# Optimization experiments

Measured on AMD Instinct MI355X. Metric: run time of the kernel, lower is better.

## Reference

```python
import jax, jax.numpy as jnp
import numpy as np

EMBED = 256; HEADS = 8; LEVELS = 4; POINTS = 4; DIM = EMBED // HEADS


def _bilinear_gather(vflat, H, W, px, py):
    """grid_sample(mode='bilinear', padding='zeros', align_corners=False).
    vflat: (bs, heads, H*W, d); px, py: (bs, heads, nq, P) pixel coords.
    Returns (bs, heads, nq, P, d).
    """
    x0 = jnp.floor(px); y0 = jnp.floor(py)
    x1 = x0 + 1.0;      y1 = y0 + 1.0
    wx1 = px - x0; wx0 = 1.0 - wx1
    wy1 = py - y0; wy0 = 1.0 - wy1

    def corner(ix, iy, w):
        valid = (ix >= 0) & (ix <= W - 1) & (iy >= 0) & (iy <= H - 1)
        idx = (jnp.clip(iy, 0, H - 1) * W + jnp.clip(ix, 0, W - 1)).astype(jnp.int32)
        b, h, nq, P = idx.shape
        g = jnp.take_along_axis(vflat, idx.reshape(b, h, nq * P)[..., None], axis=2)
        g = g.reshape(b, h, nq, P, -1)
        return g * (w * valid)[..., None]

    return (corner(x0, y0, wx0 * wy0) + corner(x1, y0, wx1 * wy0)
            + corner(x0, y1, wx0 * wy1) + corner(x1, y1, wx1 * wy1))


def _ms_deform_attn(value4, shapes, loc, attn):
    """value4 (bs,nv,heads,D); loc (bs,nq,heads,L,P,2) in [0,1];
    attn (bs,nq,heads,L,P). Returns (bs,nq,heads*D)."""
    bs, nq = loc.shape[0], loc.shape[1]
    grids = 2.0 * loc - 1.0
    attn_t = jnp.transpose(attn, (0, 2, 1, 3, 4))  # (bs,heads,nq,L,P)
    out = jnp.zeros((bs, HEADS, nq, DIM), value4.dtype)
    start = 0
    for lvl in range(LEVELS):
        H, W = int(shapes[lvl, 0]), int(shapes[lvl, 1])
        v = value4[:, start:start + H * W]                 # (bs,HW,heads,D)
        vflat = jnp.transpose(v, (0, 2, 1, 3))             # (bs,heads,HW,D)
        g = jnp.transpose(grids[:, :, :, lvl], (0, 2, 1, 3, 4))  # (bs,heads,nq,P,2)
        px = (g[..., 0] + 1.0) * (W * 0.5) - 0.5
        py = (g[..., 1] + 1.0) * (H * 0.5) - 0.5
        sampled = _bilinear_gather(vflat, H, W, px, py)    # (bs,heads,nq,P,D)
        out = out + jnp.einsum('bhqpd,bhqp->bhqd', sampled, attn_t[:, :, :, lvl])
        start += H * W
    return jnp.transpose(out, (0, 2, 1, 3)).reshape(bs, nq, HEADS * DIM)


def _forward(query, value, query_pos, reference_points, last_reference_offsets,
             shapes, Wv, bv, Wo, bo, Wa, ba, Wout, bout):
    identity = query
    q = query + query_pos
    bs, nq, _ = q.shape
    nv = value.shape[1]
    v = (value @ Wv + bv).reshape(bs, nv, HEADS, DIM)
    off = (q @ Wo + bo).reshape(bs, nq, HEADS, LEVELS, POINTS, 2)
    attn = jax.nn.softmax((q @ Wa + ba).reshape(bs, nq, HEADS, LEVELS * POINTS), axis=-1)
    attn = attn.reshape(bs, nq, HEADS, LEVELS, POINTS)
    wh = jnp.asarray(np.asarray(shapes)[:, ::-1].copy(), jnp.float32)  # (L,2) as (w,h)
    loc = (reference_points[:, :, None, :, None, :]
           + off / wh[None, None, None, :, None, :]
           + last_reference_offsets[:, :, :, None, None, :])  # flow-guided per-head shift
    out = _ms_deform_attn(v, shapes, loc, attn)
    return out @ Wout + bout + identity  # dropout is identity at eval


def setup_inputs() -> dict:
    key = jax.random.key(0)
    ks = jax.random.split(key, 10)
    bs, nq = 8, 1200
    shapes = np.array([[92, 160], [46, 80], [23, 40], [12, 20]], np.int64)
    nv = int((shapes[:, 0] * shapes[:, 1]).sum())
    f = jnp.float32
    return {
        "query": jax.random.normal(ks[0], (bs, nq, EMBED), f),
        "value": jax.random.normal(ks[1], (bs, nv, EMBED), f),
        "query_pos": jax.random.normal(ks[2], (bs, nq, EMBED), f),
        "reference_points": jax.random.uniform(ks[3], (bs, nq, LEVELS, 2), f),
        "last_reference_offsets": jax.random.normal(ks[4], (bs, nq, HEADS, 2), f) * 0.02,
        "spatial_shapes": shapes,
        "Wv": jax.random.normal(ks[5], (EMBED, EMBED), f) * 0.02,
        "bv": jnp.zeros((EMBED,), f),
        "Wo": jax.random.normal(ks[6], (EMBED, HEADS * LEVELS * POINTS * 2), f) * 0.02,
        "bo": jax.random.normal(ks[7], (HEADS * LEVELS * POINTS * 2,), f) * 0.02,
        "Wa": jax.random.normal(ks[8], (EMBED, HEADS * LEVELS * POINTS), f) * 0.02,
        "ba": jnp.zeros((HEADS * LEVELS * POINTS,), f),
        "Wout": jax.random.normal(ks[9], (EMBED, EMBED), f) * 0.02,
        "bout": jnp.zeros((EMBED,), f),
    }


def reference(query, value, query_pos, reference_points, last_reference_offsets,
              spatial_shapes, Wv, bv, Wo, bo, Wa, ba, Wout, bout):
    return _forward(query, value, query_pos, reference_points, last_reference_offsets,
                    spatial_shapes, Wv, bv, Wo, bo, Wa, ba, Wout, bout)
```

## Files before the change

### kernel.cpp

```cpp
#include <hip/hip_runtime.h>
#include <math.h>

#define BS 8
#define NQ 1200
#define NV 19560
#define NVP 19584
#define EMB 256
#define TPB 153

typedef __bf16 bf16;
typedef bf16 bf16x8 __attribute__((ext_vector_type(8)));
typedef bf16 bf16x4 __attribute__((ext_vector_type(4)));
typedef float f32x4 __attribute__((ext_vector_type(4)));

static __device__ __forceinline__ bf16x8 cvt8(float4 a, float4 b) {
    bf16x8 r;
    r[0] = (bf16)a.x; r[1] = (bf16)a.y; r[2] = (bf16)a.z; r[3] = (bf16)a.w;
    r[4] = (bf16)b.x; r[5] = (bf16)b.y; r[6] = (bf16)b.z; r[7] = (bf16)b.w;
    return r;
}

static __device__ __forceinline__ void gl16(const void* g, void* l) {
    __builtin_amdgcn_global_load_lds(
        (const __attribute__((address_space(1))) void*)g,
        (__attribute__((address_space(3))) void*)l, 16, 0, 0);
}

__global__ __launch_bounds__(256) void prep_k(
    const float* __restrict__ Wv, const float* __restrict__ Wo,
    const float* __restrict__ Wa, const float* __restrict__ Wout,
    const float* __restrict__ query, const float* __restrict__ qpos,
    const float* __restrict__ bo, const float* __restrict__ ba,
    bf16* __restrict__ Wv_p, bf16* __restrict__ Wo_p,
    bf16* __restrict__ Wa_p, bf16* __restrict__ Wout_p,
    bf16* __restrict__ qsum, float* __restrict__ cb)
{
    int bid = blockIdx.x, tid = threadIdx.x;
    if (bid < 896) {
        const float* src; bf16* dst; int N, t0;
        if (bid < 256)      { src = Wv;   dst = Wv_p;   N = 256; t0 = bid * 256; }
        else if (bid < 512) { src = Wo;   dst = Wo_p;   N = 256; t0 = (bid - 256) * 256; }
        else if (bid < 640) { src = Wa;   dst = Wa_p;   N = 128; t0 = (bid - 512) * 256; }
        else                { src = Wout; dst = Wout_p; N = 256; t0 = (bid - 640) * 256; }
        int t = t0 + tid;
        int n = t >> 8, k = t & 255;
        dst[t] = (bf16)src[k * N + n];
    } else if (bid < 10496) {
        int t = (bid - 896) * 256 + tid;
        qsum[t] = (bf16)(query[t] + qpos[t]);
    } else {
        cb[tid] = bo[tid];
        if (tid < 128) cb[256 + tid] = ba[tid];
    }
}

__global__ __launch_bounds__(256, 1) void vgemm_k(
    const float* __restrict__ A, const bf16* __restrict__ Bp,
    const float* __restrict__ bias, bf16* __restrict__ outB, int Mtiles)
{
    __shared__ __align__(16) bf16  sB[256 * 256];
    __shared__ __align__(16) float sA[4 * 2 * 1024];
    const int tid = threadIdx.x;
    const int lane = tid & 63;
    const int w = tid >> 6;
    const int l16 = lane & 15;
    const int qd = lane >> 4;

#pragma unroll
    for (int i = 0; i < 32; ++i) {
        int s = i * 256 + tid;
        int r = s >> 5, p = s & 31, c = p ^ (r & 7);
        gl16(Bp + (size_t)r * 256 + c * 8, sB + ((size_t)i * 256 + w * 64) * 8);
    }

    float* sAw = sA + w * 2048;
    const int arow = lane >> 3;
    const int aslot = (lane & 7) ^ arow;
    auto stageT = [&](int t_, int kg, int buf) {
        int b_ = t_ / TPB, p0_ = (t_ - b_ * TPB) * 128;
#pragma unroll
        for (int i = 0; i < 4; ++i) {
            int pix = min(p0_ + w * 32 + i * 8 + arow, NV - 1);
            gl16(A + ((size_t)b_ * NV + pix) * 256 + kg * 32 + aslot * 4,
                 sAw + buf * 1024 + i * 256);
        }
    };

    int t = blockIdx.x;
    stageT(t, 0, 0);
    stageT(t, 1, 1);

    f32x4 bias4[16];
#pragma unroll
    for (int ct = 0; ct < 16; ++ct)
        bias4[ct] = *(const f32x4*)(bias + ct * 16 + qd * 4);

    __syncthreads();

    const int akey = l16 & 7;
    f32x4 acc0[16], acc1[16];

    auto compute = [&](int kg, int buf) {
        const float* ab = sAw + buf * 1024;
        const float* ar0 = ab + l16 * 32;
        const float* ar1 = ab + (16 + l16) * 32;
        float4 a00 = *(const float4*)(ar0 + ((qd * 2    ) ^ akey) * 4);
        float4 a01 = *(const float4*)(ar0 + ((qd * 2 + 1) ^ akey) * 4);
        float4 a10 = *(const float4*)(ar1 + ((qd * 2    ) ^ akey) * 4);
        float4 a11 = *(const float4*)(ar1 + ((qd * 2 + 1) ^ akey) * 4);
        bf16x8 af0 = cvt8(a00, a01);
        bf16x8 af1 = cvt8(a10, a11);
#pragma unroll
        for (int ct = 0; ct < 16; ++ct) {
            int brow = ct * 16 + l16;
            bf16x8 bfr = *(const bf16x8*)(sB + (size_t)brow * 256 +
                                          ((kg * 4 + qd) ^ (brow & 7)) * 8);
            acc0[ct] = __builtin_amdgcn_mfma_f32_16x16x32_bf16(bfr, af0, acc0[ct], 0, 0, 0);
            acc1[ct] = __builtin_amdgcn_mfma_f32_16x16x32_bf16(bfr, af1, acc1[ct], 0, 0, 0);
        }
    };

#define VM_WAIT36 asm volatile("s_waitcnt vmcnt(36)" ::: "memory")
#define VM_WAIT4  asm volatile("s_waitcnt vmcnt(4)"  ::: "memory")

    while (true) {
#pragma unroll
        for (int ct = 0; ct < 16; ++ct) { acc0[ct] = bias4[ct]; acc1[ct] = bias4[ct]; }

        int tn = t + gridDim.x;
        const bool last = (tn >= Mtiles);

        VM_WAIT36; compute(0, 0); stageT(t, 2, 0);
        VM_WAIT36; compute(1, 1); stageT(t, 3, 1);
        VM_WAIT4;  compute(2, 0); stageT(t, 4, 0);
        VM_WAIT4;  compute(3, 1); stageT(t, 5, 1);
        VM_WAIT4;  compute(4, 0); stageT(t, 6, 0);
        VM_WAIT4;  compute(5, 1); stageT(t, 7, 1);
        VM_WAIT4;  compute(6, 0); if (!last) stageT(tn, 0, 0);
        VM_WAIT4;  compute(7, 1); if (!last) stageT(tn, 1, 1);

        int b = t / TPB, p0 = (t - b * TPB) * 128;
        int pix0 = p0 + w * 32 + l16;
#pragma unroll
        for (int ct = 0; ct < 16; ++ct) {
            bf16* dst = outB + ((size_t)(b * 8 + (ct >> 1)) * NVP) * 32
                             + (ct & 1) * 16 + qd * 4;
            bf16x4 v0, v1;
#pragma unroll
            for (int r = 0; r < 4; ++r) { v0[r] = (bf16)acc0[ct][r]; v1[r] = (bf16)acc1[ct][r]; }
            *(bf16x4*)(dst + (size_t)pix0 * 32)        = v0;
            *(bf16x4*)(dst + (size_t)(pix0 + 16) * 32) = v1;
        }

        if (last) break;
        t = tn;
    }
#undef VM_WAIT36
#undef VM_WAIT4
}

template <int NS, int NB, int NGRP, bool HAS_RES, bool OUT_BF16>
__global__ __launch_bounds__(256, 2) void gemm3_k(
    const bf16* __restrict__ Ah, const bf16* __restrict__ Bp,
    const float* __restrict__ bias, const float* __restrict__ res,
    float* __restrict__ outF, bf16* __restrict__ outB, int Mtiles)
{
    constexpr int CT = NB / 16;
    __shared__ __align__(16) bf16 sB[NB * 256];
    const int tid = threadIdx.x;
    const int lane = tid & 63;
    const int w = tid >> 6;
    const int l16 = lane & 15;
    const int qd = lane >> 4;
    const int col0 = (blockIdx.x % NGRP) * NB;
    const int tstride = gridDim.x / NGRP;
    const bf16* Bsrc = Bp + (size_t)col0 * 256;

    uint4 curH[8], nxtH[8];
    auto loadA = [&](int t, uint4* dH) {
        size_t rb = ((size_t)t * 64 + w * 16 + l16) * 256;
#pragma unroll
        for (int kc = 0; kc < 8; ++kc)
            dH[kc] = *(const uint4*)(Ah + rb + kc * 32 + qd * 8);
    };

    int tile = blockIdx.x / NGRP;
    if (tile < Mtiles) loadA(tile, curH);

#pragma unroll
    for (int i = 0; i < NB * 32 / 256; ++i) {
        int s = i * 256 + tid;
        int r = s >> 5, p = s & 31, c = p ^ (r & 7);
        gl16(Bsrc + (size_t)r * 256 + c * 8, sB + (size_t)(i * 256 + w * 64) * 8);
    }
    __syncthreads();

    for (; tile < Mtiles; tile += tstride) {
        int nt = tile + tstride;
        if (nt < Mtiles) loadA(nt, nxtH);

        f32x4 acc[CT];
#pragma unroll
        for (int c = 0; c < CT; ++c) acc[c] = (f32x4){0.f, 0.f, 0.f, 0.f};
#pragma unroll
        for (int kc = 0; kc < 8; ++kc) {
            bf16x8 af = *(const bf16x8*)&curH[kc];
#pragma unroll
            for (int ct = 0; ct < CT; ++ct) {
                int brow = ct * 16 + l16;
                int chunk = (kc * 4 + qd) ^ (l16 & 7);
                bf16x8 bfr = *(const bf16x8*)(sB + (size_t)brow * 256 + chunk * 8);
                acc[ct] = __builtin_amdgcn_mfma_f32_16x16x32_bf16(af, bfr, acc[ct], 0, 0, 0);
            }
        }
#pragma unroll
        for (int ct = 0; ct < CT; ++ct) {
            int col = col0 + ct * 16 + l16;
            float bbv = bias[col];
#pragma unroll
            for (int r = 0; r < 4; ++r) {
                int row = tile * 64 + w * 16 + qd * 4 + r;
                size_t idx = (size_t)row * NS + col;
                float v = acc[ct][r] + bbv;
                if (HAS_RES) v += res[(size_t)row * 256 + col];
                if (OUT_BF16) outB[idx] = (bf16)v;
                else          outF[idx] = v;
            }
        }
#pragma unroll
        for (int i = 0; i < 8; ++i) curH[i] = nxtH[i];
    }
}

static __device__ __forceinline__ void b8f(uint4 u, float* f) {
    f[0] = __uint_as_float(u.x << 16); f[1] = __uint_as_float(u.x & 0xffff0000u);
    f[2] = __uint_as_float(u.y << 16); f[3] = __uint_as_float(u.y & 0xffff0000u);
    f[4] = __uint_as_float(u.z << 16); f[5] = __uint_as_float(u.z & 0xffff0000u);
    f[6] = __uint_as_float(u.w << 16); f[7] = __uint_as_float(u.w & 0xffff0000u);
}

__global__ __launch_bounds__(256) void sample4_k(
    const bf16* __restrict__ vv, const float* __restrict__ comb,
    const float* __restrict__ refp, const float* __restrict__ lref,
    bf16* __restrict__ outb)
{
    const int cH[4] = {92, 46, 23, 12};
    const int cW[4] = {160, 80, 40, 20};
    const int cS[4] = {0, 14720, 18400, 19320};
    const int w = threadIdx.x >> 6;
    const int lane = threadIdx.x & 63;
    const int wid = blockIdx.x * 4 + w;
    const int bq = wid >> 3, h = wid & 7;
    const int b = bq / NQ;
    const int ps = lane >> 3;
    const int dg8 = lane & 7;
    const int hx2 = dg8 >> 2;

    float lg0 = comb[(size_t)bq * 384 + 256 + h * 16 + ps];
    float lg1 = comb[(size_t)bq * 384 + 256 + h * 16 + 8 + ps];
    float mx = fmaxf(lg0, lg1);
#pragma unroll
    for (int s = 8; s < 64; s <<= 1) mx = fmaxf(mx, __shfl_xor(mx, s));
    float e0 = __expf(lg0 - mx), e1 = __expf(lg1 - mx);
    float ss = e0 + e1;
#pragma unroll
    for (int s = 8; s < 64; s <<= 1) ss += __shfl_xor(ss, s);
    float inv = 1.f / ss;

    float acc[8];
#pragma unroll
    for (int j = 0; j < 8; j++) acc[j] = 0.f;

    const float* rp = refp + (size_t)bq * 8;
    float lrx = lref[(size_t)bq * 16 + h * 2];
    float lry = lref[(size_t)bq * 16 + h * 2 + 1];

#pragma unroll
    for (int s2 = 0; s2 < 2; ++s2) {
        int p = s2 * 8 + ps;
        int lvl = p >> 2;
        const int Hh = cH[lvl], Ww = cW[lvl];
        float ox = comb[(size_t)bq * 384 + h * 32 + p * 2];
        float oy = comb[(size_t)bq * 384 + h * 32 + p * 2 + 1];
        float rx = rp[lvl * 2], ry = rp[lvl * 2 + 1];

        float px = (rx + ox / (float)Ww + lrx) * (float)Ww - 0.5f;
        float py = (ry + oy / (float)Hh + lry) * (float)Hh - 0.5f;
        float x0f = floorf(px), y0f = floorf(py);
        int x0 = (int)x0f, y0 = (int)y0f;
        float wx1 = px - x0f, wx0 = 1.f - wx1;
        float wy1 = py - y0f, wy0 = 1.f - wy1;
        bool xa = (unsigned)x0 < (unsigned)Ww, xb = (unsigned)(x0 + 1) < (unsigned)Ww;
        bool ya = (unsigned)y0 < (unsigned)Hh, yb = (unsigned)(y0 + 1) < (unsigned)Hh;
        int px0 = min(max(x0, 0), Ww - 2);
        int hx = px0 + hx2;
        float wxh = (hx == x0 && xa) ? wx0 : ((hx == x0 + 1 && xb) ? wx1 : 0.f);
        int yc0 = min(max(y0, 0), Hh - 1), yc1 = min(max(y0 + 1, 0), Hh - 1);
        float wgt = (s2 ? e1 : e0) * inv;
        float wA = wgt * wy0 * (ya ? 1.f : 0.f) * wxh;
        float wB = wgt * wy1 * (yb ? 1.f : 0.f) * wxh;

        const bf16* base = vv + ((size_t)(b * 8 + h) * NVP + cS[lvl]) * 32 + dg8 * 8;
        uint4 gA = *(const uint4*)(base + ((size_t)yc0 * Ww + px0) * 32);
        uint4 gB = *(const uint4*)(base + ((size_t)yc1 * Ww + px0) * 32);

        float f[8];
        b8f(gA, f);
#pragma unroll
        for (int j = 0; j < 8; j++) acc[j] = fmaf(wA, f[j], acc[j]);
        b8f(gB, f);
#pragma unroll
        for (int j = 0; j < 8; j++) acc[j] = fmaf(wB, f[j], acc[j]);
    }

#pragma unroll
    for (int s = 4; s < 64; s <<= 1)
#pragma unroll
        for (int j = 0; j < 8; j++) acc[j] += __shfl_xor(acc[j], s);

    if (lane < 4) {
        bf16x8 o;
#pragma unroll
        for (int j = 0; j < 8; j++) o[j] = (bf16)acc[j];
        *(bf16x8*)(outb + (size_t)bq * 256 + h * 32 + lane * 8) = o;
    }
}

extern "C" void kernel_launch(void* const* d_in, const int* in_sizes, int n_in,
                              void* d_out, int out_size, void* d_ws, size_t ws_size,
                              hipStream_t stream) {
    (void)in_sizes; (void)n_in; (void)out_size; (void)ws_size;
    const float* query = (const float*)d_in[0];
    const float* value = (const float*)d_in[1];
    const float* qpos  = (const float*)d_in[2];
    const float* refp  = (const float*)d_in[3];
    const float* lref  = (const float*)d_in[4];
    const float* Wv   = (const float*)d_in[6];
    const float* bv   = (const float*)d_in[7];
    const float* Wo   = (const float*)d_in[8];
    const float* bo   = (const float*)d_in[9];
    const float* Wa   = (const float*)d_in[10];
    const float* ba   = (const float*)d_in[11];
    const float* Wout = (const float*)d_in[12];
    const float* bout = (const float*)d_in[13];

    char* ws = (char*)d_ws;
    bf16*  Wv_p   = (bf16*)(ws + 0);
    bf16*  Wo_p   = (bf16*)(ws + 131072);
    bf16*  Wa_p   = (bf16*)(ws + 262144);
    bf16*  Wout_p = (bf16*)(ws + 327680);
    bf16*  qsum   = (bf16*)(ws + 458752);
    float* comb   = (float*)(ws + 5373952);
    bf16*  tsa_b  = (bf16*)(ws + 20119552);
    bf16*  v_b    = (bf16*)(ws + 25034752);
    float* cbias  = (float*)(ws + 105250816);

    prep_k<<<10497, 256, 0, stream>>>(Wv, Wo, Wa, Wout, query, qpos, bo, ba,
                                      Wv_p, Wo_p, Wa_p, Wout_p, qsum, cbias);

    vgemm_k<<<256, 256, 0, stream>>>(value, Wv_p, bv, v_b, BS * TPB);
    gemm3_k<384, 128, 3, false, false><<<450, 256, 0, stream>>>(
        qsum, Wo_p, cbias, nullptr, comb, nullptr, (BS * NQ) / 64);
    sample4_k<<<(BS * NQ * 8) / 4, 256, 0, stream>>>(v_b, comb, refp, lref, tsa_b);
    gemm3_k<256, 128, 2, true, false><<<300, 256, 0, stream>>>(
        tsa_b, Wout_p, bout, query, (float*)d_out, nullptr, (BS * NQ) / 64);
}
```

Baseline: 393.2 us.

## Replace persistent value GEMM with per-tile K-chunked blocks and tiled weight transpose

Measured after the change: 399.2 us. No clear change (+1.5%).

```diff
diff --git a/kernel.cpp b/kernel.cpp
--- a/kernel.cpp
+++ b/kernel.cpp
@@ -35,128 +35,135 @@
     bf16* __restrict__ Wa_p, bf16* __restrict__ Wout_p,
     bf16* __restrict__ qsum, float* __restrict__ cb)
 {
+    __shared__ float t64[64][65];
     int bid = blockIdx.x, tid = threadIdx.x;
-    if (bid < 896) {
-        const float* src; bf16* dst; int N, t0;
-        if (bid < 256)      { src = Wv;   dst = Wv_p;   N = 256; t0 = bid * 256; }
-        else if (bid < 512) { src = Wo;   dst = Wo_p;   N = 256; t0 = (bid - 256) * 256; }
-        else if (bid < 640) { src = Wa;   dst = Wa_p;   N = 128; t0 = (bid - 512) * 256; }
-        else                { src = Wout; dst = Wout_p; N = 256; t0 = (bid - 640) * 256; }
-        int t = t0 + tid;
-        int n = t >> 8, k = t & 255;
-        dst[t] = (bf16)src[k * N + n];
-    } else if (bid < 10496) {
-        int t = (bid - 896) * 256 + tid;
-        qsum[t] = (bf16)(query[t] + qpos[t]);
+    if (bid < 56) {
+        const float* src; bf16* dst; int N, tile;
+        if (bid < 16)      { src = Wv;   dst = Wv_p;   N = 256; tile = bid; }
+        else if (bid < 32) { src = Wo;   dst = Wo_p;   N = 256; tile = bid - 16; }
+        else if (bid < 40) { src = Wa;   dst = Wa_p;   N = 128; tile = bid - 32; }
+        else               { src = Wout; dst = Wout_p; N = 256; tile = bid - 40; }
+        int ntn = N >> 6;
+        int k0 = (tile / ntn) << 6, n0 = (tile % ntn) << 6;
+#pragma unroll
+        for (int j = 0; j < 16; ++j) {
+            int idx = j * 256 + tid;
+            int r = idx >> 6, c = idx & 63;
+            t64[r][c] = src[(size_t)(k0 + r) * N + n0 + c];
+        }
+        __syncthreads();
+#pragma unroll
+        for (int j = 0; j < 16; ++j) {
+            int idx = j * 256 + tid;
+            int rn = idx >> 6, ck = idx & 63;
+            dst[(size_t)(n0 + rn) * 256 + k0 + ck] = (bf16)t64[ck][rn];
+        }
+    } else if (bid < 1256) {
+        size_t base = (size_t)(bid - 56) * 2048 + tid * 8;
+        float4 a0 = *(const float4*)(query + base);
+        float4 a1 = *(const float4*)(query + base + 4);
+        float4 b0 = *(const float4*)(qpos + base);
+        float4 b1 = *(const float4*)(qpos + base + 4);
+        bf16x8 o;
+        o[0] = (bf16)(a0.x + b0.x); o[1] = (bf16)(a0.y + b0.y);
+        o[2] = (bf16)(a0.z + b0.z); o[3] = (bf16)(a0.w + b0.w);
+        o[4] = (bf16)(a1.x + b1.x); o[5] = (bf16)(a1.y + b1.y);
+        o[6] = (bf16)(a1.z + b1.z); o[7] = (bf16)(a1.w + b1.w);
+        *(bf16x8*)(qsum + base) = o;
     } else {
         cb[tid] = bo[tid];
         if (tid < 128) cb[256 + tid] = ba[tid];
     }
 }
 
-__global__ __launch_bounds__(256, 1) void vgemm_k(
+__global__ __launch_bounds__(256, 2) void vgemm_k(
     const float* __restrict__ A, const bf16* __restrict__ Bp,
-    const float* __restrict__ bias, bf16* __restrict__ outB, int Mtiles)
+    const float* __restrict__ bias, bf16* __restrict__ outB)
 {
-    __shared__ __align__(16) bf16  sB[256 * 256];
-    __shared__ __align__(16) float sA[4 * 2 * 1024];
+    __shared__ __align__(16) float sA[2][128 * 32];
+    __shared__ __align__(16) bf16  sB[2][256 * 32];
     const int tid = threadIdx.x;
     const int lane = tid & 63;
     const int w = tid >> 6;
     const int l16 = lane & 15;
     const int qd = lane >> 4;
-
-#pragma unroll
-    for (int i = 0; i < 32; ++i) {
-        int s = i * 256 + tid;
-        int r = s >> 5, p = s & 31, c = p ^ (r & 7);
-        gl16(Bp + (size_t)r * 256 + c * 8, sB + ((size_t)i * 256 + w * 64) * 8);
-    }
-
-    float* sAw = sA + w * 2048;
+    const int t = blockIdx.x;
+    const int b = t / TPB, p0 = (t - b * TPB) * 128;
+
     const int arow = lane >> 3;
-    const int aslot = (lane & 7) ^ arow;
-    auto stageT = [&](int t_, int kg, int buf) {
-        int b_ = t_ / TPB, p0_ = (t_ - b_ * TPB) * 128;
+    const int aslot = lane & 7;
+    auto stageA = [&](int kg, int buf) {
 #pragma unroll
         for (int i = 0; i < 4; ++i) {
-            int pix = min(p0_ + w * 32 + i * 8 + arow, NV - 1);
-            gl16(A + ((size_t)b_ * NV + pix) * 256 + kg * 32 + aslot * 4,
-                 sAw + buf * 1024 + i * 256);
+            int lr = w * 32 + i * 8 + arow;
+            int pix = min(p0 + lr, NV - 1);
+            int gs = aslot ^ arow;
+            gl16(A + ((size_t)b * NV + pix) * 256 + kg * 32 + gs * 4,
+                 (float*)sA[buf] + (w * 32 + i * 8) * 32);
         }
     };
-
-    int t = blockIdx.x;
-    stageT(t, 0, 0);
-    stageT(t, 1, 1);
-
-    f32x4 bias4[16];
-#pragma unroll
-    for (int ct = 0; ct < 16; ++ct)
-        bias4[ct] = *(const f32x4*)(bias + ct * 16 + qd * 4);
+    const int bcol = lane >> 2;
+    const int bslt = lane & 3;
+    auto stageB = [&](int kg, int buf) {
+#pragma unroll
+        for (int i = 0; i < 4; ++i) {
+            int c = w * 64 + i * 16 + bcol;
+            int key = (c ^ (c >> 2)) & 3;
+            gl16(Bp + (size_t)c * 256 + kg * 32 + (bslt ^ key) * 8,
+                 (bf16*)sB[buf] + (w * 64 + i * 16) * 32);
+        }
+    };
+
+    stageA(0, 0);
+    stageB(0, 0);
+
+    f32x4 acc0[16], acc1[16];
+#pragma unroll
+    for (int ct = 0; ct < 16; ++ct) {
+        f32x4 bb = *(const f32x4*)(bias + ct * 16 + qd * 4);
+        acc0[ct] = bb; acc1[ct] = bb;
+    }
 
     __syncthreads();
 
     const int akey = l16 & 7;
-    f32x4 acc0[16], acc1[16];
-
-    auto compute = [&](int kg, int buf) {
-        const float* ab = sAw + buf * 1024;
-        const float* ar0 = ab + l16 * 32;
-        const float* ar1 = ab + (16 + l16) * 32;
-        float4 a00 = *(const float4*)(ar0 + ((qd * 2    ) ^ akey) * 4);
-        float4 a01 = *(const float4*)(ar0 + ((qd * 2 + 1) ^ akey) * 4);
-        float4 a10 = *(const float4*)(ar1 + ((qd * 2    ) ^ akey) * 4);
-        float4 a11 = *(const float4*)(ar1 + ((qd * 2 + 1) ^ akey) * 4);
-        bf16x8 af0 = cvt8(a00, a01);
-        bf16x8 af1 = cvt8(a10, a11);
-#pragma unroll
-        for (int ct = 0; ct < 16; ++ct) {
-            int brow = ct * 16 + l16;
-            bf16x8 bfr = *(const bf16x8*)(sB + (size_t)brow * 256 +
-                                          ((kg * 4 + qd) ^ (brow & 7)) * 8);
-            acc0[ct] = __builtin_amdgcn_mfma_f32_16x16x32_bf16(bfr, af0, acc0[ct], 0, 0, 0);
-            acc1[ct] = __builtin_amdgcn_mfma_f32_16x16x32_bf16(bfr, af1, acc1[ct], 0, 0, 0);
-        }
-    };
-
-#define VM_WAIT36 asm volatile("s_waitcnt vmcnt(36)" ::: "memory")
-#define VM_WAIT4  asm volatile("s_waitcnt vmcnt(4)"  ::: "memory")
-
-    while (true) {
-#pragma unroll
-        for (int ct = 0; ct < 16; ++ct) { acc0[ct] = bias4[ct]; acc1[ct] = bias4[ct]; }
-
-        int tn = t + gridDim.x;
-        const bool last = (tn >= Mtiles);
-
-        VM_WAIT36; compute(0, 0); stageT(t, 2, 0);
-        VM_WAIT36; compute(1, 1); stageT(t, 3, 1);
-        VM_WAIT4;  compute(2, 0); stageT(t, 4, 0);
-        VM_WAIT4;  compute(3, 1); stageT(t, 5, 1);
-        VM_WAIT4;  compute(4, 0); stageT(t, 6, 0);
-        VM_WAIT4;  compute(5, 1); stageT(t, 7, 1);
-        VM_WAIT4;  compute(6, 0); if (!last) stageT(tn, 0, 0);
-        VM_WAIT4;  compute(7, 1); if (!last) stageT(tn, 1, 1);
-
-        int b = t / TPB, p0 = (t - b * TPB) * 128;
-        int pix0 = p0 + w * 32 + l16;
-#pragma unroll
-        for (int ct = 0; ct < 16; ++ct) {
-            bf16* dst = outB + ((size_t)(b * 8 + (ct >> 1)) * NVP) * 32
-                             + (ct & 1) * 16 + qd * 4;
-            bf16x4 v0, v1;
-#pragma unroll
-            for (int r = 0; r < 4; ++r) { v0[r] = (bf16)acc0[ct][r]; v1[r] = (bf16)acc1[ct][r]; }
-            *(bf16x4*)(dst + (size_t)pix0 * 32)        = v0;
-            *(bf16x4*)(dst + (size_t)(pix0 + 16) * 32) = v1;
-        }
-
-        if (last) break;
-        t = tn;
-    }
-#undef VM_WAIT36
-#undef VM_WAIT4
+    int buf = 0;
+#pragma unroll
+    for (int kc = 0; kc < 8; ++kc) {
+        if (kc < 7) { stageA(kc + 1, buf ^ 1); stageB(kc + 1, buf ^ 1); }
+        {
+            const float* ar0 = sA[buf] + (w * 32 + l16) * 32;
+            const float* ar1 = ar0 + 16 * 32;
+            float4 a00 = *(const float4*)(ar0 + ((qd * 2    ) ^ akey) * 4);
+            float4 a01 = *(const float4*)(ar0 + ((qd * 2 + 1) ^ akey) * 4);
+            float4 a10 = *(const float4*)(ar1 + ((qd * 2    ) ^ akey) * 4);
+            float4 a11 = *(const float4*)(ar1 + ((qd * 2 + 1) ^ akey) * 4);
+            bf16x8 af0 = cvt8(a00, a01);
+            bf16x8 af1 = cvt8(a10, a11);
+#pragma unroll
+            for (int ct = 0; ct < 16; ++ct) {
+                int c = ct * 16 + l16;
+                int key = (c ^ (c >> 2)) & 3;
+                bf16x8 bfr = *(const bf16x8*)(sB[buf] + (size_t)c * 32 + (qd ^ key) * 8);
+                acc0[ct] = __builtin_amdgcn_mfma_f32_16x16x32_bf16(bfr, af0, acc0[ct], 0, 0, 0);
+                acc1[ct] = __builtin_amdgcn_mfma_f32_16x16x32_bf16(bfr, af1, acc1[ct], 0, 0, 0);
+            }
+        }
+        __syncthreads();
+        buf ^= 1;
+    }
+
+    int pix0 = p0 + w * 32 + l16;
+#pragma unroll
+    for (int ct = 0; ct < 16; ++ct) {
+        bf16* dst = outB + ((size_t)(b * 8 + (ct >> 1)) * NVP) * 32
+                         + (ct & 1) * 16 + qd * 4;
+        bf16x4 v0, v1;
+#pragma unroll
+        for (int r = 0; r < 4; ++r) { v0[r] = (bf16)acc0[ct][r]; v1[r] = (bf16)acc1[ct][r]; }
+        *(bf16x4*)(dst + (size_t)pix0 * 32)        = v0;
+        *(bf16x4*)(dst + (size_t)(pix0 + 16) * 32) = v1;
+    }
 }
 
 template <int NS, int NB, int NGRP, bool HAS_RES, bool OUT_BF16>
@@ -355,10 +362,10 @@
     bf16*  v_b    = (bf16*)(ws + 25034752);
     float* cbias  = (float*)(ws + 105250816);
 
-    prep_k<<<10497, 256, 0, stream>>>(Wv, Wo, Wa, Wout, query, qpos, bo, ba,
-                                      Wv_p, Wo_p, Wa_p, Wout_p, qsum, cbias);
-
-    vgemm_k<<<256, 256, 0, stream>>>(value, Wv_p, bv, v_b, BS * TPB);
+    prep_k<<<1257, 256, 0, stream>>>(Wv, Wo, Wa, Wout, query, qpos, bo, ba,
+                                     Wv_p, Wo_p, Wa_p, Wout_p, qsum, cbias);
+
+    vgemm_k<<<BS * TPB, 256, 0, stream>>>(value, Wv_p, bv, v_b);
     gemm3_k<384, 128, 3, false, false><<<450, 256, 0, stream>>>(
         qsum, Wo_p, cbias, nullptr, comb, nullptr, (BS * NQ) / 64);
     sample4_k<<<(BS * NQ * 8) / 4, 256, 0, stream>>>(v_b, comb, refp, lref, tsa_b);
```
